# Performance work log

Hardware: AMD Instinct MI355X
Metric: run time of the kernel (lower is better)

Reference implementation:

```python
import jax, jax.numpy as jnp
import numpy as np

B_, T, N, C = 1024, 8, 49, 96
NUM_HEADS = 3
NW = 64  # number of distinct window masks


def setup_inputs() -> dict:
    key = jax.random.key(0)
    ks = jax.random.split(key, 8)
    x = jax.random.normal(ks[0], (B_, T, N, C), dtype=jnp.float32)
    # Swin-style additive mask: mostly 0, some large-negative entries
    mask = jnp.where(jax.random.uniform(ks[1], (NW, N, N)) < 0.9, 0.0, -100.0).astype(jnp.float32)
    s = 0.02
    qkv_w = jax.random.normal(ks[2], (C, 3 * C), dtype=jnp.float32) * s
    qkv_b = jnp.zeros((3 * C,), dtype=jnp.float32)
    proj_sp_w = jax.random.normal(ks[3], (C, C), dtype=jnp.float32) * s
    proj_sp_b = jnp.zeros((C,), dtype=jnp.float32)
    proj_temp_w = jax.random.normal(ks[4], (C, C), dtype=jnp.float32) * s
    proj_temp_b = jnp.zeros((C,), dtype=jnp.float32)
    return {
        "x": x, "mask": mask,
        "qkv_w": qkv_w, "qkv_b": qkv_b,
        "proj_sp_w": proj_sp_w, "proj_sp_b": proj_sp_b,
        "proj_temp_w": proj_temp_w, "proj_temp_b": proj_temp_b,
    }


def _attend(xseq, qkv_w, qkv_b, num_heads, scale, mask=None):
    """xseq: (B, L, C). Returns (B, L, C). mask: (nW, L, L) or None."""
    Bt, L, Cd = xseq.shape
    hd = Cd // num_heads
    qkv = (xseq @ qkv_w + qkv_b).reshape(Bt, L, 3, num_heads, hd)
    q, k, v = qkv[:, :, 0], qkv[:, :, 1], qkv[:, :, 2]  # (B, L, H, hd)
    attn = jnp.einsum("bnhd,bmhd->bhnm", q * scale, k)  # (B, H, L, L)
    if mask is not None:
        nW = mask.shape[0]
        attn = attn.reshape(Bt // nW, nW, num_heads, L, L) + mask[None, :, None]
        attn = attn.reshape(Bt, num_heads, L, L)
    attn = jax.nn.softmax(attn, axis=-1)
    out = jnp.einsum("bhnm,bmhd->bnhd", attn, v).reshape(Bt, L, Cd)
    return out


def reference(x, mask, qkv_w, qkv_b, proj_sp_w, proj_sp_b, proj_temp_w, proj_temp_b):
    Bw, Tt, Nn, Cc = x.shape
    hd = Cc // NUM_HEADS
    scale = hd ** (-0.5)
    # spatial branch: attention over N within each (window, time)
    x_sp = _attend(x.reshape(Bw * Tt, Nn, Cc), qkv_w, qkv_b, NUM_HEADS, scale, mask)
    x_sp = (x_sp @ proj_sp_w + proj_sp_b).reshape(Bw, Tt, Nn, Cc)
    # temporal branch: attention over T for each spatial token
    x_t = x.transpose(0, 2, 1, 3).reshape(Bw * Nn, Tt, Cc)
    x_t = _attend(x_t, qkv_w, qkv_b, NUM_HEADS, scale, None)
    x_t = (x_t @ proj_temp_w + proj_temp_b)
    x_t = x_t.reshape(Bw, Nn, Tt, Cc).transpose(0, 2, 1, 3)
    return (x_t, x_sp)
```

## Files before the change

kernel.cpp:

```cpp
#include <hip/hip_runtime.h>

typedef __bf16 bf16x2 __attribute__((ext_vector_type(2)));
typedef __bf16 bf16x4 __attribute__((ext_vector_type(4)));
typedef __bf16 bf16x8 __attribute__((ext_vector_type(8)));
typedef float f32x4 __attribute__((ext_vector_type(4)));
#define MFMA __builtin_amdgcn_mfma_f32_16x16x32_bf16

#define SCALE 0.17677669529663687f
#define QS2 200
#define QS3 296
#define VS 72
#define PS 72
#define CS 104

__device__ __forceinline__ bf16x4 cvt4(const float* p) {
  bf16x4 v;
  float4 f = *(const float4*)p;
  v[0] = (__bf16)f.x; v[1] = (__bf16)f.y; v[2] = (__bf16)f.z; v[3] = (__bf16)f.w;
  return v;
}
__device__ __forceinline__ bf16x4 bz4() {
  bf16x4 z;
  for (int i = 0; i < 4; ++i) z[i] = (__bf16)0.f;
  return z;
}

__global__ __launch_bounds__(256) void k_transpose(const float* __restrict__ Wq,
    const float* __restrict__ Wsp, const float* __restrict__ Wtm,
    __bf16* __restrict__ ws) {
  const int which = blockIdx.x, tid = threadIdx.x;
  if (which == 0) {
    for (int idx = tid; idx < 27648; idx += 256) {
      int n = idx / 96, k = idx % 96;
      ws[idx] = (__bf16)Wq[k * 288 + n];
    }
  } else {
    const float* src = (which == 1) ? Wsp : Wtm;
    __bf16* dst = ws + 27648 + (which - 1) * 9216;
    for (int idx = tid; idx < 9216; idx += 256) {
      int n = idx / 96, k = idx % 96;
      dst[idx] = (__bf16)src[k * 96 + n];
    }
  }
}

__global__ __launch_bounds__(256) void k_spatial(const float* __restrict__ x,
    const __bf16* __restrict__ WqT, const float* __restrict__ qkv_b,
    const float* __restrict__ mask, const __bf16* __restrict__ WpT,
    const float* __restrict__ bp, float* __restrict__ out) {
  __shared__ __align__(16) char smem[67072];
  __bf16* qk  = (__bf16*)(smem);
  __bf16* ctx = (__bf16*)(smem);
  __bf16* xt  = (__bf16*)(smem + 25600);
  __bf16* P   = (__bf16*)(smem + 25600);
  __bf16* VT  = (__bf16*)(smem + 53248);

  const int tid = threadIdx.x;
  const int bt = blockIdx.x;
  const long rbase = (long)bt * 49;
  const int wave = tid >> 6, lane = tid & 63, lr = lane & 15, quad = lane >> 4;

  const float* xg = x + rbase * 96;
  for (int v = tid; v < 1536; v += 256) {
    int r = v / 24, c = (v % 24) * 4;
    bf16x4 val = bz4();
    if (r < 49) val = cvt4(&xg[r * 96 + c]);
    *(bf16x4*)&xt[r * CS + c] = val;
  }
  __syncthreads();
  {
    bf16x8 afr[4][3];
    for (int rt = 0; rt < 4; ++rt)
      for (int ks = 0; ks < 3; ++ks)
        afr[rt][ks] = *(const bf16x8*)&xt[(rt * 16 + lr) * CS + ks * 32 + quad * 8];
    for (int ct = wave; ct < 18; ct += 4) {
      const __bf16* wrow = &WqT[(ct * 16 + lr) * 96 + quad * 8];
      bf16x8 b0 = *(const bf16x8*)&wrow[0];
      bf16x8 b1 = *(const bf16x8*)&wrow[32];
      bf16x8 b2 = *(const bf16x8*)&wrow[64];
      int col = ct * 16 + lr;
      float bv = qkv_b[col];
      for (int rt = 0; rt < 4; ++rt) {
        f32x4 acc = {0.f, 0.f, 0.f, 0.f};
        acc = MFMA(afr[rt][0], b0, acc, 0, 0, 0);
        acc = MFMA(afr[rt][1], b1, acc, 0, 0, 0);
        acc = MFMA(afr[rt][2], b2, acc, 0, 0, 0);
        if (ct < 12) {
          for (int i = 0; i < 4; ++i)
            qk[(rt * 16 + quad * 4 + i) * QS2 + col] = (__bf16)(acc[i] + bv);
        } else {
          int d = col - 192;
          __bf16* vp = &VT[d * VS + rt * 16 + quad * 4];
          bf16x2 lo; lo[0] = (__bf16)(acc[0] + bv); lo[1] = (__bf16)(acc[1] + bv);
          bf16x2 hi; hi[0] = (__bf16)(acc[2] + bv); hi[1] = (__bf16)(acc[3] + bv);
          *(bf16x2*)&vp[0] = lo;
          *(bf16x2*)&vp[2] = hi;
        }
      }
    }
  }
  __syncthreads();

  {
    const int rt = wave;
    const int nb = rt * 16 + quad * 4;
    const float* mrow = mask + (long)(bt & 63) * 2401;
    for (int h = 0; h < 3; ++h) {
      bf16x8 qf = *(const bf16x8*)&qk[(rt * 16 + lr) * QS2 + h * 32 + quad * 8];
      float sv[4][4];
      for (int ct = 0; ct < 4; ++ct) {
        bf16x8 kf = *(const bf16x8*)&qk[(ct * 16 + lr) * QS2 + 96 + h * 32 + quad * 8];
        f32x4 acc = {0.f, 0.f, 0.f, 0.f};
        acc = MFMA(qf, kf, acc, 0, 0, 0);
        int m = ct * 16 + lr;
        int mm = (m < 49) ? m : 48;
        for (int i = 0; i < 4; ++i) {
          int nn = (nb + i < 49) ? nb + i : 48;
          float mv = mrow[nn * 49 + mm];
          sv[ct][i] = (m < 49) ? (acc[i] * SCALE + mv) : -1e30f;
        }
      }
      for (int i = 0; i < 4; ++i) {
        float mx = fmaxf(fmaxf(sv[0][i], sv[1][i]), fmaxf(sv[2][i], sv[3][i]));
        mx = fmaxf(mx, __shfl_xor(mx, 1));
        mx = fmaxf(mx, __shfl_xor(mx, 2));
        mx = fmaxf(mx, __shfl_xor(mx, 4));
        mx = fmaxf(mx, __shfl_xor(mx, 8));
        float e0 = __expf(sv[0][i] - mx), e1 = __expf(sv[1][i] - mx);
        float e2 = __expf(sv[2][i] - mx), e3 = __expf(sv[3][i] - mx);
        float sum = e0 + e1 + e2 + e3;
        sum += __shfl_xor(sum, 1);
        sum += __shfl_xor(sum, 2);
        sum += __shfl_xor(sum, 4);
        sum += __shfl_xor(sum, 8);
        float inv = 1.f / sum;
        __bf16* Pr = &P[(h * 64 + nb + i) * PS + lr];
        Pr[0]  = (__bf16)(e0 * inv);
        Pr[16] = (__bf16)(e1 * inv);
        Pr[32] = (__bf16)(e2 * inv);
        Pr[48] = (__bf16)(e3 * inv);
      }
    }
  }
  __syncthreads();

  for (int tile = wave; tile < 24; tile += 4) {
    int h = tile / 8, rt = (tile / 2) & 3, dt = tile & 1;
    f32x4 acc = {0.f, 0.f, 0.f, 0.f};
    for (int ks = 0; ks < 2; ++ks) {
      bf16x8 a  = *(const bf16x8*)&P[(h * 64 + rt * 16 + lr) * PS + ks * 32 + quad * 8];
      bf16x8 bb = *(const bf16x8*)&VT[(h * 32 + dt * 16 + lr) * VS + ks * 32 + quad * 8];
      acc = MFMA(a, bb, acc, 0, 0, 0);
    }
    for (int i = 0; i < 4; ++i)
      ctx[(rt * 16 + quad * 4 + i) * CS + h * 32 + dt * 16 + lr] = (__bf16)acc[i];
  }
  __syncthreads();

  for (int tile = wave; tile < 24; tile += 4) {
    int rt = tile / 6, ct = tile % 6;
    int col = ct * 16 + lr;
    const __bf16* wrow = &WpT[col * 96 + quad * 8];
    f32x4 acc = {0.f, 0.f, 0.f, 0.f};
    for (int ks = 0; ks < 3; ++ks) {
      bf16x8 a  = *(const bf16x8*)&ctx[(rt * 16 + lr) * CS + ks * 32 + quad * 8];
      bf16x8 bb = *(const bf16x8*)&wrow[ks * 32];
      acc = MFMA(a, bb, acc, 0, 0, 0);
    }
    float bv = bp[col];
    for (int i = 0; i < 4; ++i) {
      int r = rt * 16 + quad * 4 + i;
      if (r < 49) out[(rbase + r) * 96 + col] = acc[i] + bv;
    }
  }
}

__global__ __launch_bounds__(256) void k_temporal(const float* __restrict__ x,
    const __bf16* __restrict__ WqT, const float* __restrict__ qkv_b,
    const __bf16* __restrict__ WpT, const float* __restrict__ bp,
    float* __restrict__ out) {
  __shared__ __align__(16) char smem[51200];
  __bf16* qk  = (__bf16*)(smem);
  __bf16* xt  = (__bf16*)(smem + 37888);
  __bf16* ctx = (__bf16*)(smem + 37888);

  const int tid = threadIdx.x;
  const int n0 = blockIdx.x * 8;
  const int b = blockIdx.y;
  const int wave = tid >> 6, lane = tid & 63, lr = lane & 15, quad = lane >> 4;

  for (int v = tid; v < 1536; v += 256) {
    int r = v / 24, c = (v % 24) * 4;
    int t = r >> 3, n = n0 + (r & 7);
    bf16x4 val = bz4();
    if (n < 49) val = cvt4(&x[((long)(b * 8 + t) * 49 + n) * 96 + c]);
    *(bf16x4*)&xt[r * CS + c] = val;
  }
  __syncthreads();
  {
    bf16x8 afr[4][3];
    for (int rt = 0; rt < 4; ++rt)
      for (int ks = 0; ks < 3; ++ks)
        afr[rt][ks] = *(const bf16x8*)&xt[(rt * 16 + lr) * CS + ks * 32 + quad * 8];
    for (int ct = wave; ct < 18; ct += 4) {
      const __bf16* wrow = &WqT[(ct * 16 + lr) * 96 + quad * 8];
      bf16x8 b0 = *(const bf16x8*)&wrow[0];
      bf16x8 b1 = *(const bf16x8*)&wrow[32];
      bf16x8 b2 = *(const bf16x8*)&wrow[64];
      int col = ct * 16 + lr;
      float bv = qkv_b[col];
      for (int rt = 0; rt < 4; ++rt) {
        f32x4 acc = {0.f, 0.f, 0.f, 0.f};
        acc = MFMA(afr[rt][0], b0, acc, 0, 0, 0);
        acc = MFMA(afr[rt][1], b1, acc, 0, 0, 0);
        acc = MFMA(afr[rt][2], b2, acc, 0, 0, 0);
        for (int i = 0; i < 4; ++i)
          qk[(rt * 16 + quad * 4 + i) * QS3 + col] = (__bf16)(acc[i] + bv);
      }
    }
  }
  __syncthreads();

  if (tid < 192) {
    int ni = tid & 7, h = (tid >> 3) % 3, i = tid / 24;
    const int ro = h * 32;
    float q[32];
    for (int d = 0; d < 32; ++d) q[d] = (float)qk[(i * 8 + ni) * QS3 + ro + d];
    float s[8], mx = -1e30f;
    for (int j = 0; j < 8; ++j) {
      const __bf16* kr = &qk[(j * 8 + ni) * QS3 + 96 + ro];
      float acc = 0.f;
      for (int d = 0; d < 32; ++d) acc += q[d] * (float)kr[d];
      acc *= SCALE;
      s[j] = acc; mx = fmaxf(mx, acc);
    }
    float sum = 0.f;
    for (int j = 0; j < 8; ++j) { s[j] = __expf(s[j] - mx); sum += s[j]; }
    float inv = 1.f / sum;
    float o[32];
    for (int d = 0; d < 32; ++d) o[d] = 0.f;
    for (int j = 0; j < 8; ++j) {
      float p = s[j] * inv;
      const __bf16* vr = &qk[(j * 8 + ni) * QS3 + 192 + ro];
      for (int d = 0; d < 32; ++d) o[d] += p * (float)vr[d];
    }
    for (int d = 0; d < 32; ++d) ctx[(i * 8 + ni) * CS + ro + d] = (__bf16)o[d];
  }
  __syncthreads();

  for (int tile = wave; tile < 24; tile += 4) {
    int rt = tile / 6, ct = tile % 6;
    int col = ct * 16 + lr;
    const __bf16* wrow = &WpT[col * 96 + quad * 8];
    f32x4 acc = {0.f, 0.f, 0.f, 0.f};
    for (int ks = 0; ks < 3; ++ks) {
      bf16x8 a  = *(const bf16x8*)&ctx[(rt * 16 + lr) * CS + ks * 32 + quad * 8];
      bf16x8 bb = *(const bf16x8*)&wrow[ks * 32];
      acc = MFMA(a, bb, acc, 0, 0, 0);
    }
    float bv = bp[col];
    for (int i = 0; i < 4; ++i) {
      int r = rt * 16 + quad * 4 + i;
      int t = r >> 3, n = n0 + (r & 7);
      if (n < 49) out[((long)(b * 8 + t) * 49 + n) * 96 + col] = acc[i] + bv;
    }
  }
}

extern "C" void kernel_launch(void* const* d_in, const int* in_sizes, int n_in,
                              void* d_out, int out_size, void* d_ws, size_t ws_size,
                              hipStream_t stream) {
  const float* x         = (const float*)d_in[0];
  const float* mask      = (const float*)d_in[1];
  const float* qkv_w     = (const float*)d_in[2];
  const float* qkv_b     = (const float*)d_in[3];
  const float* proj_sp_w = (const float*)d_in[4];
  const float* proj_sp_b = (const float*)d_in[5];
  const float* proj_t_w  = (const float*)d_in[6];
  const float* proj_t_b  = (const float*)d_in[7];
  float* out = (float*)d_out;
  __bf16* wsb = (__bf16*)d_ws;

  const __bf16* WqT  = wsb;
  const __bf16* WspT = wsb + 27648;
  const __bf16* WtmT = wsb + 36864;

  k_transpose<<<dim3(3), dim3(256), 0, stream>>>(qkv_w, proj_sp_w, proj_t_w, wsb);
  k_spatial<<<dim3(8192), dim3(256), 0, stream>>>(x, WqT, qkv_b, mask, WspT,
                                                  proj_sp_b, out + 38535168);
  k_temporal<<<dim3(7, 1024), dim3(256), 0, stream>>>(x, WqT, qkv_b, WtmT,
                                                      proj_t_b, out);
}
```

Measured before the change: 815.5 us.

## Use 512-thread blocks and MFMA block-diagonal attention for temporal branch

Both attention kernels now run with 8 waves per block and split the per-head softmax and matmul tiles across more waves. The spatial kernel hoists the mask loads out of the head loop so they happen once per thread. The temporal kernel reorders rows so each sequence's 8 time steps are contiguous, then computes QK^T and PV with MFMA over 16-row tiles holding two sequences, masking the off-diagonal blocks to zero. This replaces the scalar per-thread temporal attention at the cost of wasted MFMA work on those zeroed blocks, higher LDS use per block and possibly lower occupancy.

```diff
diff --git a/kernel.cpp b/kernel.cpp
--- a/kernel.cpp
+++ b/kernel.cpp
@@ -8,7 +8,6 @@
 
 #define SCALE 0.17677669529663687f
 #define QS2 200
-#define QS3 296
 #define VS 72
 #define PS 72
 #define CS 104
@@ -44,7 +43,7 @@
   }
 }
 
-__global__ __launch_bounds__(256) void k_spatial(const float* __restrict__ x,
+__global__ __launch_bounds__(512, 4) void k_spatial(const float* __restrict__ x,
     const __bf16* __restrict__ WqT, const float* __restrict__ qkv_b,
     const float* __restrict__ mask, const __bf16* __restrict__ WpT,
     const float* __restrict__ bp, float* __restrict__ out) {
@@ -61,7 +60,7 @@
   const int wave = tid >> 6, lane = tid & 63, lr = lane & 15, quad = lane >> 4;
 
   const float* xg = x + rbase * 96;
-  for (int v = tid; v < 1536; v += 256) {
+  for (int v = tid; v < 1536; v += 512) {
     int r = v / 24, c = (v % 24) * 4;
     bf16x4 val = bz4();
     if (r < 49) val = cvt4(&xg[r * 96 + c]);
@@ -73,7 +72,7 @@
     for (int rt = 0; rt < 4; ++rt)
       for (int ks = 0; ks < 3; ++ks)
         afr[rt][ks] = *(const bf16x8*)&xt[(rt * 16 + lr) * CS + ks * 32 + quad * 8];
-    for (int ct = wave; ct < 18; ct += 4) {
+    for (int ct = wave; ct < 18; ct += 8) {
       const __bf16* wrow = &WqT[(ct * 16 + lr) * 96 + quad * 8];
       bf16x8 b0 = *(const bf16x8*)&wrow[0];
       bf16x8 b1 = *(const bf16x8*)&wrow[32];
@@ -102,10 +101,20 @@
   __syncthreads();
 
   {
-    const int rt = wave;
+    const int rt = wave & 3;
     const int nb = rt * 16 + quad * 4;
     const float* mrow = mask + (long)(bt & 63) * 2401;
-    for (int h = 0; h < 3; ++h) {
+    float mv[4][4];
+    for (int ct = 0; ct < 4; ++ct) {
+      int m = ct * 16 + lr;
+      int mm = (m < 49) ? m : 48;
+      for (int i = 0; i < 4; ++i) {
+        int nn = (nb + i < 49) ? nb + i : 48;
+        mv[ct][i] = mrow[nn * 49 + mm];
+      }
+    }
+    for (int task = wave; task < 12; task += 8) {
+      int h = task >> 2;
       bf16x8 qf = *(const bf16x8*)&qk[(rt * 16 + lr) * QS2 + h * 32 + quad * 8];
       float sv[4][4];
       for (int ct = 0; ct < 4; ++ct) {
@@ -113,12 +122,8 @@
         f32x4 acc = {0.f, 0.f, 0.f, 0.f};
         acc = MFMA(qf, kf, acc, 0, 0, 0);
         int m = ct * 16 + lr;
-        int mm = (m < 49) ? m : 48;
-        for (int i = 0; i < 4; ++i) {
-          int nn = (nb + i < 49) ? nb + i : 48;
-          float mv = mrow[nn * 49 + mm];
-          sv[ct][i] = (m < 49) ? (acc[i] * SCALE + mv) : -1e30f;
-        }
+        for (int i = 0; i < 4; ++i)
+          sv[ct][i] = (m < 49) ? (acc[i] * SCALE + mv[ct][i]) : -1e30f;
       }
       for (int i = 0; i < 4; ++i) {
         float mx = fmaxf(fmaxf(sv[0][i], sv[1][i]), fmaxf(sv[2][i], sv[3][i]));
@@ -144,7 +149,7 @@
   }
   __syncthreads();
 
-  for (int tile = wave; tile < 24; tile += 4) {
+  for (int tile = wave; tile < 24; tile += 8) {
     int h = tile / 8, rt = (tile / 2) & 3, dt = tile & 1;
     f32x4 acc = {0.f, 0.f, 0.f, 0.f};
     for (int ks = 0; ks < 2; ++ks) {
@@ -157,7 +162,7 @@
   }
   __syncthreads();
 
-  for (int tile = wave; tile < 24; tile += 4) {
+  for (int tile = wave; tile < 24; tile += 8) {
     int rt = tile / 6, ct = tile % 6;
     int col = ct * 16 + lr;
     const __bf16* wrow = &WpT[col * 96 + quad * 8];
@@ -175,26 +180,28 @@
   }
 }
 
-__global__ __launch_bounds__(256) void k_temporal(const float* __restrict__ x,
+__global__ __launch_bounds__(512, 4) void k_temporal(const float* __restrict__ x,
     const __bf16* __restrict__ WqT, const float* __restrict__ qkv_b,
     const __bf16* __restrict__ WpT, const float* __restrict__ bp,
     float* __restrict__ out) {
-  __shared__ __align__(16) char smem[51200];
+  __shared__ __align__(16) char smem[67072];
   __bf16* qk  = (__bf16*)(smem);
-  __bf16* xt  = (__bf16*)(smem + 37888);
-  __bf16* ctx = (__bf16*)(smem + 37888);
+  __bf16* ctx = (__bf16*)(smem);
+  __bf16* xt  = (__bf16*)(smem + 25600);
+  __bf16* P   = (__bf16*)(smem + 25600);
+  __bf16* VT  = (__bf16*)(smem + 53248);
 
   const int tid = threadIdx.x;
   const int n0 = blockIdx.x * 8;
   const int b = blockIdx.y;
   const int wave = tid >> 6, lane = tid & 63, lr = lane & 15, quad = lane >> 4;
 
-  for (int v = tid; v < 1536; v += 256) {
-    int r = v / 24, c = (v % 24) * 4;
-    int t = r >> 3, n = n0 + (r & 7);
+  for (int v = tid; v < 1536; v += 512) {
+    int s = v / 24, c = (v % 24) * 4;
+    int ni = s >> 3, t = s & 7, n = n0 + ni;
     bf16x4 val = bz4();
     if (n < 49) val = cvt4(&x[((long)(b * 8 + t) * 49 + n) * 96 + c]);
-    *(bf16x4*)&xt[r * CS + c] = val;
+    *(bf16x4*)&xt[s * CS + c] = val;
   }
   __syncthreads();
   {
@@ -202,7 +209,7 @@
     for (int rt = 0; rt < 4; ++rt)
       for (int ks = 0; ks < 3; ++ks)
         afr[rt][ks] = *(const bf16x8*)&xt[(rt * 16 + lr) * CS + ks * 32 + quad * 8];
-    for (int ct = wave; ct < 18; ct += 4) {
+    for (int ct = wave; ct < 18; ct += 8) {
       const __bf16* wrow = &WqT[(ct * 16 + lr) * 96 + quad * 8];
       bf16x8 b0 = *(const bf16x8*)&wrow[0];
       bf16x8 b1 = *(const bf16x8*)&wrow[32];
@@ -214,41 +221,62 @@
         acc = MFMA(afr[rt][0], b0, acc, 0, 0, 0);
         acc = MFMA(afr[rt][1], b1, acc, 0, 0, 0);
         acc = MFMA(afr[rt][2], b2, acc, 0, 0, 0);
-        for (int i = 0; i < 4; ++i)
-          qk[(rt * 16 + quad * 4 + i) * QS3 + col] = (__bf16)(acc[i] + bv);
-      }
-    }
-  }
-  __syncthreads();
-
-  if (tid < 192) {
-    int ni = tid & 7, h = (tid >> 3) % 3, i = tid / 24;
-    const int ro = h * 32;
-    float q[32];
-    for (int d = 0; d < 32; ++d) q[d] = (float)qk[(i * 8 + ni) * QS3 + ro + d];
-    float s[8], mx = -1e30f;
-    for (int j = 0; j < 8; ++j) {
-      const __bf16* kr = &qk[(j * 8 + ni) * QS3 + 96 + ro];
-      float acc = 0.f;
-      for (int d = 0; d < 32; ++d) acc += q[d] * (float)kr[d];
-      acc *= SCALE;
-      s[j] = acc; mx = fmaxf(mx, acc);
-    }
-    float sum = 0.f;
-    for (int j = 0; j < 8; ++j) { s[j] = __expf(s[j] - mx); sum += s[j]; }
-    float inv = 1.f / sum;
-    float o[32];
-    for (int d = 0; d < 32; ++d) o[d] = 0.f;
-    for (int j = 0; j < 8; ++j) {
-      float p = s[j] * inv;
-      const __bf16* vr = &qk[(j * 8 + ni) * QS3 + 192 + ro];
-      for (int d = 0; d < 32; ++d) o[d] += p * (float)vr[d];
-    }
-    for (int d = 0; d < 32; ++d) ctx[(i * 8 + ni) * CS + ro + d] = (__bf16)o[d];
-  }
-  __syncthreads();
-
-  for (int tile = wave; tile < 24; tile += 4) {
+        if (ct < 12) {
+          for (int i = 0; i < 4; ++i)
+            qk[(rt * 16 + quad * 4 + i) * QS2 + col] = (__bf16)(acc[i] + bv);
+        } else {
+          int d = col - 192;
+          __bf16* vp = &VT[d * VS + rt * 16 + quad * 4];
+          bf16x2 lo; lo[0] = (__bf16)(acc[0] + bv); lo[1] = (__bf16)(acc[1] + bv);
+          bf16x2 hi; hi[0] = (__bf16)(acc[2] + bv); hi[1] = (__bf16)(acc[3] + bv);
+          *(bf16x2*)&vp[0] = lo;
+          *(bf16x2*)&vp[2] = hi;
+        }
+      }
+    }
+  }
+  __syncthreads();
+
+  {
+    const bool useful = (((lane & 15) >> 3) == (lane >> 5));
+    for (int task = wave; task < 12; task += 8) {
+      int p = task & 3, h = task >> 2;
+      bf16x8 qf = *(const bf16x8*)&qk[(p * 16 + lr) * QS2 + h * 32 + quad * 8];
+      bf16x8 kf = *(const bf16x8*)&qk[(p * 16 + lr) * QS2 + 96 + h * 32 + quad * 8];
+      f32x4 acc = {0.f, 0.f, 0.f, 0.f};
+      acc = MFMA(qf, kf, acc, 0, 0, 0);
+      for (int rr = 0; rr < 4; ++rr) {
+        float s = acc[rr] * SCALE;
+        float mx = s;
+        mx = fmaxf(mx, __shfl_xor(mx, 1));
+        mx = fmaxf(mx, __shfl_xor(mx, 2));
+        mx = fmaxf(mx, __shfl_xor(mx, 4));
+        float e = __expf(s - mx);
+        float sum = e;
+        sum += __shfl_xor(sum, 1);
+        sum += __shfl_xor(sum, 2);
+        sum += __shfl_xor(sum, 4);
+        float pv = useful ? (e / sum) : 0.f;
+        int row = h * 64 + p * 16 + quad * 4 + rr;
+        P[row * PS + p * 16 + (lane & 15)] = (__bf16)pv;
+        P[row * PS + (p ^ 1) * 16 + (lane & 15)] = (__bf16)0.f;
+      }
+    }
+  }
+  __syncthreads();
+
+  for (int task = wave; task < 24; task += 8) {
+    int h = task >> 3, pt = (task >> 1) & 3, dh = task & 1;
+    bf16x8 a  = *(const bf16x8*)&P[(h * 64 + pt * 16 + lr) * PS + (pt >> 1) * 32 + quad * 8];
+    bf16x8 bb = *(const bf16x8*)&VT[(h * 32 + dh * 16 + lr) * VS + (pt >> 1) * 32 + quad * 8];
+    f32x4 acc = {0.f, 0.f, 0.f, 0.f};
+    acc = MFMA(a, bb, acc, 0, 0, 0);
+    for (int i = 0; i < 4; ++i)
+      ctx[(pt * 16 + quad * 4 + i) * CS + h * 32 + dh * 16 + lr] = (__bf16)acc[i];
+  }
+  __syncthreads();
+
+  for (int tile = wave; tile < 24; tile += 8) {
     int rt = tile / 6, ct = tile % 6;
     int col = ct * 16 + lr;
     const __bf16* wrow = &WpT[col * 96 + quad * 8];
@@ -260,8 +288,8 @@
     }
     float bv = bp[col];
     for (int i = 0; i < 4; ++i) {
-      int r = rt * 16 + quad * 4 + i;
-      int t = r >> 3, n = n0 + (r & 7);
+      int s = rt * 16 + quad * 4 + i;
+      int t = s & 7, n = n0 + (s >> 3);
       if (n < 49) out[((long)(b * 8 + t) * 49 + n) * 96 + col] = acc[i] + bv;
     }
   }
@@ -286,8 +314,8 @@
   const __bf16* WtmT = wsb + 36864;
 
   k_transpose<<<dim3(3), dim3(256), 0, stream>>>(qkv_w, proj_sp_w, proj_t_w, wsb);
-  k_spatial<<<dim3(8192), dim3(256), 0, stream>>>(x, WqT, qkv_b, mask, WspT,
+  k_spatial<<<dim3(8192), dim3(512), 0, stream>>>(x, WqT, qkv_b, mask, WspT,
                                                   proj_sp_b, out + 38535168);
-  k_temporal<<<dim3(7, 1024), dim3(256), 0, stream>>>(x, WqT, qkv_b, WtmT,
+  k_temporal<<<dim3(7, 1024), dim3(512), 0, stream>>>(x, WqT, qkv_b, WtmT,
                                                       proj_t_b, out);
 }
```

New measurement: 665.2 us. -18.4%, faster.
